# Kernel tuning notes

Hardware: AMD Instinct MI355X
Metric: run time of the kernel (lower is better)

The kernel has to match this reference:

```python
import jax, jax.numpy as jnp
import numpy as np

L_LAYERS = 4
B = 8
PATCH_H = 37
PATCH_W = 37
P = PATCH_H * PATCH_W  # 1369
D = 1024
J = 768
H = 518
W = 518
R_LIST = [1, 3, 5]
K_LIST = [1, 2, 3]
TOPMIN_MIN = 0.0
TOPMIN_MAX = 0.3


def setup_inputs() -> dict:
    key = jax.random.key(0)
    k1, k2 = jax.random.split(key)
    features = jax.random.normal(k1, (L_LAYERS, B, P, D), dtype=jnp.float32)
    cls_tokens = jax.random.normal(k2, (B, J), dtype=jnp.float32)
    return {"features": features, "cls_tokens": cls_tokens}


def _layer_norm_2d(x, eps=1e-5):
    # torch.layer_norm with normalized_shape = (P, D): normalize jointly over last two dims, no affine
    mu = jnp.mean(x, axis=(-2, -1), keepdims=True)
    var = jnp.var(x, axis=(-2, -1), keepdims=True)
    return (x - mu) * jax.lax.rsqrt(var + eps)


def _lnamd(features, r):
    # LNAMD: unfold(r,r, zero pad r//2) + adaptive_avg_pool1d(D*r*r -> D) == per-channel r x r
    # neighborhood mean over the patch grid with zero padding (pool bins are exactly r*r wide).
    if r == 1:
        return features
    l, b, p, d = features.shape
    x = features.reshape(l * b, PATCH_H, PATCH_W, d)
    pad = r // 2
    s = jax.lax.reduce_window(x, 0.0, jax.lax.add, (1, r, r, 1), (1, 1, 1, 1),
                              [(0, 0), (pad, pad), (pad, pad), (0, 0)])
    return (s / float(r * r)).reshape(l, b, p, d)


def _msm(rf, use_remat=False):
    # rf: [L,B,P,D] L2-normalized. Mutual scoring: for each image i, euclidean cdist of its
    # patches to all other images' patches, min over ref patches, mean of [k_min:k_max] smallest.
    l, b, p, d = rf.shape
    k_min = int(TOPMIN_MIN * (b - 1))
    k_max = int(TOPMIN_MAX * (b - 1))
    sq = jnp.sum(rf * rf, axis=-1)  # [L,B,P]

    def per_image(i):
        feat = rf[:, i]  # [L,P,D]
        dots = jnp.einsum('lpd,lbqd->lpbq', feat, rf)  # [L,P,B,P]
        d2 = sq[:, i][:, :, None, None] + sq[:, None, :, :] - 2.0 * dots
        dist = jnp.sqrt(jnp.maximum(d2, 1e-12))
        mind = jnp.min(dist, axis=-1)  # [L,P,B]
        mind = jnp.where(jnp.arange(b)[None, None, :] == i, jnp.inf, mind)  # exclude self
        neg_top = jax.lax.top_k(-mind, k_max)[0]  # k_max smallest distances (ascending)
        sel = -neg_top[..., k_min:k_max]
        return jnp.mean(sel, axis=-1)  # [L,P]

    fn = jax.checkpoint(per_image) if use_remat else per_image
    scores = jax.lax.map(fn, jnp.arange(b))  # [B,L,P]; lax.map keeps one cdist block live at a time
    return jnp.transpose(scores, (1, 0, 2))  # [L,B,P]


def _rscin(sim, scores, top_k):
    # zero out the B-top_k smallest similarities per row (keep top_k largest), row-normalize, reweight
    b = sim.shape[0]
    if top_k < b:
        vals, idx = jax.lax.top_k(sim, top_k)
        masked = jnp.zeros_like(sim).at[jnp.arange(b)[:, None], idx].set(vals)
    else:
        masked = sim
    masked = masked / jnp.sum(masked, axis=-1, keepdims=True)
    return masked @ scores


def _interp_mat(out_len, in_len):
    # bilinear, align_corners=True: src = dst * (in-1)/(out-1); separable 1D interpolation matrix
    pos = jnp.arange(out_len, dtype=jnp.float32) * ((in_len - 1) / (out_len - 1))
    i0 = jnp.clip(jnp.floor(pos).astype(jnp.int32), 0, in_len - 1)
    i1 = jnp.minimum(i0 + 1, in_len - 1)
    w = pos - i0.astype(jnp.float32)
    m = jnp.zeros((out_len, in_len), jnp.float32)
    m = m.at[jnp.arange(out_len), i0].add(1.0 - w)
    m = m.at[jnp.arange(out_len), i1].add(w)
    return m


def _forward(features, cls_tokens, use_remat=False):
    feats = _layer_norm_2d(features)  # [L,B,P,D]
    per_r = []
    for r in R_LIST:
        rf = _lnamd(feats, r)
        rf = rf / jnp.linalg.norm(rf, axis=-1, keepdims=True)
        per_r.append(jnp.mean(_msm(rf, use_remat), axis=0))  # mean over layers -> [B,P]
    scores = jnp.mean(jnp.stack(per_r, axis=0), axis=0)  # [B,P]
    img_scores = jnp.max(scores, axis=1)  # [B]
    cls = cls_tokens / jnp.linalg.norm(cls_tokens, axis=-1, keepdims=True)
    sim = cls @ cls.T  # [B,B]
    final = jnp.mean(jnp.stack([_rscin(sim, img_scores, k) for k in K_LIST], axis=0), axis=0)
    patch = scores.reshape(-1, PATCH_H, PATCH_W)
    mh = _interp_mat(H, PATCH_H)
    mw = _interp_mat(W, PATCH_W)
    pixel = jnp.einsum('Hh,bhw,Ww->bHW', mh, patch, mw)  # [B,H,W]
    return final, pixel


def reference(features, cls_tokens):
    return _forward(features, cls_tokens)
```

## Files before the change

kernel.cpp:

```cpp
#include <hip/hip_runtime.h>
#include <hip/hip_bf16.h>
#include <math.h>

#define L_LAYERS 4
#define BIMG 8
#define PATCH_H 37
#define PATCH_W 37
#define PP 1369
#define DD 1024
#define JJ 768
#define HOUT 518
#define WOUT 518
#define PPAD 1408
#define NPAIR 28

typedef __bf16 bf16x8 __attribute__((ext_vector_type(8)));
typedef float floatx4 __attribute__((ext_vector_type(4)));

__device__ __forceinline__ unsigned short f2bf(float f) {
  unsigned int u = __float_as_uint(f);
  u = u + 0x7fffu + ((u >> 16) & 1u);
  return (unsigned short)(u >> 16);
}

__device__ __forceinline__ void gload_lds16(const unsigned short* gptr,
                                            unsigned short* lptr) {
  __builtin_amdgcn_global_load_lds(
      (const __attribute__((address_space(1))) unsigned int*)gptr,
      (__attribute__((address_space(3))) unsigned int*)lptr, 16, 0, 0);
}

__global__ __launch_bounds__(256) void k1_mu(const float* __restrict__ x,
                                             float* __restrict__ mu_acc) {
  const int lb = blockIdx.y;
  const float* base = x + (size_t)lb * PP * DD;
  const int N4 = PP * DD / 4;
  float s = 0.0f;
  for (int idx = blockIdx.x * 256 + threadIdx.x; idx < N4; idx += gridDim.x * 256) {
    float4 u = *(const float4*)(base + (size_t)idx * 4);
    s += u.x + u.y + u.z + u.w;
  }
  for (int off = 1; off < 64; off <<= 1) s += __shfl_xor(s, off, 64);
  __shared__ float red[4];
  if ((threadIdx.x & 63) == 0) red[threadIdx.x >> 6] = s;
  __syncthreads();
  if (threadIdx.x == 0)
    atomicAdd(&mu_acc[lb], red[0] + red[1] + red[2] + red[3]);
}

__global__ __launch_bounds__(256) void k2_pool(const float* __restrict__ x,
                                               const float* __restrict__ mu_acc,
                                               unsigned short* __restrict__ rf,
                                               int r) {
  const int p  = blockIdx.x;
  const int lb = blockIdx.y;
  const int tid = threadIdx.x;
  const int d0 = tid * 4;
  const size_t outbase = ((size_t)lb * PPAD + p) * DD;
  if (p >= PP) {
    ushort4 z; z.x = 0; z.y = 0; z.z = 0; z.w = 0;
    *(ushort4*)(rf + outbase + d0) = z;
    return;
  }
  const float mu = mu_acc[lb] * (1.0f / ((float)PP * (float)DD));
  const int ph = p / PATCH_W, pw = p % PATCH_W;
  const int pad = r >> 1;
  float s0 = 0, s1 = 0, s2 = 0, s3 = 0;
  int cnt = 0;
  for (int dy = -pad; dy <= pad; dy++) {
    int qh = ph + dy; if (qh < 0 || qh >= PATCH_H) continue;
    for (int dx = -pad; dx <= pad; dx++) {
      int qw = pw + dx; if (qw < 0 || qw >= PATCH_W) continue;
      cnt++;
      const float* src = x + ((size_t)lb * PP + qh * PATCH_W + qw) * DD + d0;
      float4 u = *(const float4*)src;
      s0 += u.x; s1 += u.y; s2 += u.z; s3 += u.w;
    }
  }
  const float cm = (float)cnt * mu;
  s0 -= cm; s1 -= cm; s2 -= cm; s3 -= cm;
  float sq = s0 * s0 + s1 * s1 + s2 * s2 + s3 * s3;
  for (int off = 1; off < 64; off <<= 1) sq += __shfl_xor(sq, off, 64);
  __shared__ float red[4];
  if ((tid & 63) == 0) red[tid >> 6] = sq;
  __syncthreads();
  const float tot = red[0] + red[1] + red[2] + red[3];
  const float rn = rsqrtf(tot);
  ushort4 o;
  o.x = f2bf(s0 * rn); o.y = f2bf(s1 * rn); o.z = f2bf(s2 * rn); o.w = f2bf(s3 * rn);
  *(ushort4*)(rf + outbase + d0) = o;
}

__global__ __launch_bounds__(256) void k3_pairdots(const unsigned short* __restrict__ rf,
                                                   unsigned int* __restrict__ mind) {
  const int l = blockIdx.z / NPAIR;
  int rem = blockIdx.z % NPAIR;
  int i = 0, span = BIMG - 1;
  while (rem >= span) { rem -= span; span--; i++; }
  const int j = i + 1 + rem;

  const int rowbase = blockIdx.x * 128;
  const int colbase = blockIdx.y * 128;
  const unsigned short* A  = rf + ((size_t)(l * BIMG + i) * PPAD + rowbase) * DD;
  const unsigned short* Bp = rf + ((size_t)(l * BIMG + j) * PPAD + colbase) * DD;

  __shared__ __align__(16) unsigned short lA[128 * 32];
  __shared__ __align__(16) unsigned short lB[128 * 32];

  const int tid  = threadIdx.x;
  const int lane = tid & 63;
  const int wave = tid >> 6;
  const int lrow = lane & 15;
  const int quad = lane >> 4;
  const int wr = (wave >> 1) * 64;
  const int wc = (wave & 1) * 64;

  floatx4 acc[4][4];
#pragma unroll
  for (int a = 0; a < 4; a++)
#pragma unroll
    for (int b = 0; b < 4; b++) acc[a][b] = (floatx4){0.f, 0.f, 0.f, 0.f};

  const int srow   = wave * 32 + (lane >> 2);
  const int schunk = (lane & 3) * 8;
  const unsigned short* gA0 = A  + (size_t)srow * DD + schunk;
  const unsigned short* gA1 = gA0 + (size_t)16 * DD;
  const unsigned short* gB0 = Bp + (size_t)srow * DD + schunk;
  const unsigned short* gB1 = gB0 + (size_t)16 * DD;
  unsigned short* lA0 = lA + wave * 1024;
  unsigned short* lB0 = lB + wave * 1024;

  for (int k0 = 0; k0 < DD; k0 += 32) {
    __syncthreads();
    gload_lds16(gA0 + k0, lA0);
    gload_lds16(gA1 + k0, lA0 + 512);
    gload_lds16(gB0 + k0, lB0);
    gload_lds16(gB1 + k0, lB0 + 512);
    __syncthreads();
    bf16x8 af[4], bfv[4];
#pragma unroll
    for (int mt = 0; mt < 4; mt++)
      af[mt] = *(const bf16x8*)(lA + (wr + mt * 16 + lrow) * 32 + quad * 8);
#pragma unroll
    for (int ct = 0; ct < 4; ct++)
      bfv[ct] = *(const bf16x8*)(lB + (wc + ct * 16 + lrow) * 32 + quad * 8);
#pragma unroll
    for (int mt = 0; mt < 4; mt++)
#pragma unroll
      for (int ct = 0; ct < 4; ct++)
        acc[mt][ct] = __builtin_amdgcn_mfma_f32_16x16x32_bf16(af[mt], bfv[ct],
                                                              acc[mt][ct], 0, 0, 0);
  }

  unsigned int* mrow = mind + ((size_t)(l * BIMG + i) * BIMG + j) * PP;
  unsigned int* mcol = mind + ((size_t)(l * BIMG + j) * BIMG + i) * PP;

#pragma unroll
  for (int mt = 0; mt < 4; mt++) {
#pragma unroll
    for (int reg = 0; reg < 4; reg++) {
      const int gr = rowbase + wr + mt * 16 + quad * 4 + reg;
      float v = -1e30f;
#pragma unroll
      for (int ct = 0; ct < 4; ct++) {
        const int gc = colbase + wc + ct * 16 + lrow;
        if (gc < PP) v = fmaxf(v, acc[mt][ct][reg]);
      }
      for (int off = 1; off < 16; off <<= 1) v = fmaxf(v, __shfl_xor(v, off, 64));
      if (lrow == 0 && gr < PP && v > -1e29f)
        atomicMax(mrow + gr, __float_as_uint(v + 2.0f));
    }
  }
#pragma unroll
  for (int ct = 0; ct < 4; ct++) {
    const int gc = colbase + wc + ct * 16 + lrow;
    float v = -1e30f;
#pragma unroll
    for (int mt = 0; mt < 4; mt++) {
      const int grb = rowbase + wr + mt * 16 + quad * 4;
#pragma unroll
      for (int reg = 0; reg < 4; reg++)
        if (grb + reg < PP) v = fmaxf(v, acc[mt][ct][reg]);
    }
    for (int off = 16; off < 64; off <<= 1) v = fmaxf(v, __shfl_xor(v, off, 64));
    if (quad == 0 && gc < PP && v > -1e29f)
      atomicMax(mcol + gc, __float_as_uint(v + 2.0f));
  }
}

__global__ void k4_scores(const unsigned int* __restrict__ mind,
                          float* __restrict__ scores) {
  const int idx = blockIdx.x * 256 + threadIdx.x;
  if (idx >= BIMG * PP) return;
  const int i = idx / PP, p = idx % PP;
  float accum = 0.0f;
  for (int l = 0; l < L_LAYERS; l++) {
    float m1 = 1e30f, m2 = 1e30f;
    for (int b = 0; b < BIMG; b++) {
      if (b == i) continue;
      const unsigned int enc = mind[((size_t)(l * BIMG + i) * BIMG + b) * PP + p];
      const float dot = __uint_as_float(enc) - 2.0f;
      const float d2 = fmaxf(2.0f - 2.0f * dot, 1e-12f);
      const float dist = sqrtf(d2);
      if (dist < m1) { m2 = m1; m1 = dist; }
      else if (dist < m2) { m2 = dist; }
    }
    accum += 0.5f * (m1 + m2);
  }
  scores[idx] += accum * (1.0f / (float)(L_LAYERS * 3));
}

__global__ void k5_imgmax(const float* __restrict__ scores, float* __restrict__ img) {
  const int i = blockIdx.x;
  float m = -1e30f;
  for (int p = threadIdx.x; p < PP; p += 256) m = fmaxf(m, scores[i * PP + p]);
  for (int off = 1; off < 64; off <<= 1) m = fmaxf(m, __shfl_xor(m, off, 64));
  __shared__ float red[4];
  if ((threadIdx.x & 63) == 0) red[threadIdx.x >> 6] = m;
  __syncthreads();
  if (threadIdx.x == 0)
    img[i] = fmaxf(fmaxf(red[0], red[1]), fmaxf(red[2], red[3]));
}

__global__ void k6_final(const float* __restrict__ cls,
                         const float* __restrict__ img,
                         float* __restrict__ out) {
  __shared__ float norms[BIMG];
  __shared__ float sim[BIMG][BIMG];
  const int t = threadIdx.x;
  if (t < BIMG) {
    float s = 0;
    for (int d = 0; d < JJ; d++) { float v = cls[t * JJ + d]; s += v * v; }
    norms[t] = sqrtf(s);
  }
  __syncthreads();
  {
    const int ii = t >> 3, jj = t & 7;
    float s = 0;
    for (int d = 0; d < JJ; d++) s += cls[ii * JJ + d] * cls[jj * JJ + d];
    sim[ii][jj] = s / (norms[ii] * norms[jj]);
  }
  __syncthreads();
  if (t < BIMG) {
    float v[8]; int id[8];
    for (int a = 0; a < 8; a++) { v[a] = sim[t][a]; id[a] = a; }
    for (int a = 0; a < 8; a++) {
      int best = a;
      for (int b = a + 1; b < 8; b++) if (v[b] > v[best]) best = b;
      float tv = v[a]; v[a] = v[best]; v[best] = tv;
      int ti = id[a]; id[a] = id[best]; id[best] = ti;
    }
    float res = 0;
    for (int k = 1; k <= 3; k++) {
      float num = 0, den = 0;
      for (int a = 0; a < k; a++) { num += v[a] * img[id[a]]; den += v[a]; }
      res += num / den;
    }
    out[t] = res * (1.0f / 3.0f);
  }
}

__global__ void k7_pixel(const float* __restrict__ scores,
                         float* __restrict__ out) {
  const int idx = blockIdx.x * 256 + threadIdx.x;
  if (idx >= BIMG * HOUT * WOUT) return;
  const int b = idx / (HOUT * WOUT);
  const int rem = idx % (HOUT * WOUT);
  const int Y = rem / WOUT, X = rem % WOUT;
  const float sy = (float)(PATCH_H - 1) / (float)(HOUT - 1);
  const float sx = (float)(PATCH_W - 1) / (float)(WOUT - 1);
  float py = (float)Y * sy;
  float px = (float)X * sx;
  int y0 = (int)floorf(py); y0 = min(max(y0, 0), PATCH_H - 1);
  int x0 = (int)floorf(px); x0 = min(max(x0, 0), PATCH_W - 1);
  const int y1 = min(y0 + 1, PATCH_H - 1);
  const int x1 = min(x0 + 1, PATCH_W - 1);
  const float wy = py - (float)y0, wx = px - (float)x0;
  const float* sc = scores + (size_t)b * PP;
  const float v =
      (1.f - wy) * ((1.f - wx) * sc[y0 * PATCH_W + x0] + wx * sc[y0 * PATCH_W + x1]) +
      wy         * ((1.f - wx) * sc[y1 * PATCH_W + x0] + wx * sc[y1 * PATCH_W + x1]);
  out[8 + idx] = v;
}

extern "C" void kernel_launch(void* const* d_in, const int* in_sizes, int n_in,
                              void* d_out, int out_size, void* d_ws, size_t ws_size,
                              hipStream_t stream) {
  const float* feat = (const float*)d_in[0];
  const float* cls  = (const float*)d_in[1];
  float* out = (float*)d_out;

  char* ws = (char*)d_ws;
  size_t off = 0;
  unsigned short* rf = (unsigned short*)(ws + off);
  off += (size_t)L_LAYERS * BIMG * PPAD * DD * 2;
  unsigned int* mind = (unsigned int*)(ws + off);
  off += (size_t)L_LAYERS * BIMG * BIMG * PP * 4;
  float* scores = (float*)(ws + off);
  off += (size_t)BIMG * PP * 4;
  float* mu_acc = (float*)(ws + off);
  off += 32 * 4;
  float* img = (float*)(ws + off);
  off += 8 * 4;

  hipMemsetAsync(mu_acc, 0, 32 * 4, stream);
  hipMemsetAsync(scores, 0, (size_t)BIMG * PP * 4, stream);
  k1_mu<<<dim3(43, 32), 256, 0, stream>>>(feat, mu_acc);

  const int rlist[3] = {1, 3, 5};
  for (int ri = 0; ri < 3; ri++) {
    k2_pool<<<dim3(PPAD, 32), 256, 0, stream>>>(feat, mu_acc, rf, rlist[ri]);
    hipMemsetAsync(mind, 0, (size_t)L_LAYERS * BIMG * BIMG * PP * 4, stream);
    k3_pairdots<<<dim3(11, 11, L_LAYERS * NPAIR), 256, 0, stream>>>(rf, mind);
    k4_scores<<<(BIMG * PP + 255) / 256, 256, 0, stream>>>(mind, scores);
  }
  k5_imgmax<<<8, 256, 0, stream>>>(scores, img);
  k6_final<<<1, 64, 0, stream>>>(cls, img, out);
  k7_pixel<<<(BIMG * HOUT * WOUT + 255) / 256, 256, 0, stream>>>(scores, out);
}
```

Measured before the change: 2.927 ms.

## Quantize normalized features to FP8 e4m3 and use fp8 MFMA for pair dots

Normalized pooled features are now stored as FP8 e4m3, scaled by 16, instead of bf16. The Gram-matrix kernel uses fp8 MFMA with 64-wide K steps and XOR-swizzled LDS. Each row's quantized squared norm is stored, so distances are rebuilt as n_i + n_j - 2dot from the actual quantized values. This halves feature bandwidth and LDS traffic and doubles MFMA throughput, at the cost of lower precision in the nearest-neighbour distances.

New measurement: 2.594 ms. -11.4%, faster.

```diff
diff --git a/kernel.cpp b/kernel.cpp
--- a/kernel.cpp
+++ b/kernel.cpp
@@ -14,17 +14,31 @@
 #define PPAD 1408
 #define NPAIR 28
 
-typedef __bf16 bf16x8 __attribute__((ext_vector_type(8)));
 typedef float floatx4 __attribute__((ext_vector_type(4)));
 
-__device__ __forceinline__ unsigned short f2bf(float f) {
-  unsigned int u = __float_as_uint(f);
-  u = u + 0x7fffu + ((u >> 16) & 1u);
-  return (unsigned short)(u >> 16);
-}
-
-__device__ __forceinline__ void gload_lds16(const unsigned short* gptr,
-                                            unsigned short* lptr) {
+__device__ __forceinline__ unsigned int f2e4m3(float v) {
+  unsigned int b = __float_as_uint(v);
+  unsigned int sign = (b >> 24) & 0x80u;
+  float mag = fabsf(v);
+  unsigned int code;
+  if (mag >= 0.015625f) {
+    unsigned int mb = __float_as_uint(mag);
+    mb = mb + 0x0007ffffu + ((mb >> 20) & 1u);
+    code = (((mb >> 23) - 120u) << 3) | ((mb >> 20) & 7u);
+  } else {
+    code = (unsigned int)__float2int_rn(mag * 512.0f);
+  }
+  return code | sign;
+}
+__device__ __forceinline__ float e4m3tof(unsigned int c) {
+  unsigned int em = c & 0x7fu;
+  float m;
+  if (em >= 8u) m = __uint_as_float((((em >> 3) + 120u) << 23) | ((em & 7u) << 20));
+  else          m = (float)em * 0.001953125f;
+  return (c & 0x80u) ? -m : m;
+}
+
+__device__ __forceinline__ void gload_lds16(const void* gptr, void* lptr) {
   __builtin_amdgcn_global_load_lds(
       (const __attribute__((address_space(1))) unsigned int*)gptr,
       (__attribute__((address_space(3))) unsigned int*)lptr, 16, 0, 0);
@@ -50,7 +64,8 @@
 
 __global__ __launch_bounds__(256) void k2_pool(const float* __restrict__ x,
                                                const float* __restrict__ mu_acc,
-                                               unsigned short* __restrict__ rf,
+                                               unsigned char* __restrict__ rf,
+                                               float* __restrict__ nrm,
                                                int r) {
   const int p  = blockIdx.x;
   const int lb = blockIdx.y;
@@ -58,8 +73,9 @@
   const int d0 = tid * 4;
   const size_t outbase = ((size_t)lb * PPAD + p) * DD;
   if (p >= PP) {
-    ushort4 z; z.x = 0; z.y = 0; z.z = 0; z.w = 0;
-    *(ushort4*)(rf + outbase + d0) = z;
+    uchar4 z; z.x = 0; z.y = 0; z.z = 0; z.w = 0;
+    *(uchar4*)(rf + outbase + d0) = z;
+    if (tid == 0) nrm[(size_t)lb * PPAD + p] = 0.0f;
     return;
   }
   const float mu = mu_acc[lb] * (1.0f / ((float)PP * (float)DD));
@@ -84,14 +100,24 @@
   __shared__ float red[4];
   if ((tid & 63) == 0) red[tid >> 6] = sq;
   __syncthreads();
-  const float tot = red[0] + red[1] + red[2] + red[3];
-  const float rn = rsqrtf(tot);
-  ushort4 o;
-  o.x = f2bf(s0 * rn); o.y = f2bf(s1 * rn); o.z = f2bf(s2 * rn); o.w = f2bf(s3 * rn);
-  *(ushort4*)(rf + outbase + d0) = o;
-}
-
-__global__ __launch_bounds__(256) void k3_pairdots(const unsigned short* __restrict__ rf,
+  const float rn16 = rsqrtf(red[0] + red[1] + red[2] + red[3]) * 16.0f;
+  unsigned int c0 = f2e4m3(s0 * rn16), c1 = f2e4m3(s1 * rn16);
+  unsigned int c2 = f2e4m3(s2 * rn16), c3 = f2e4m3(s3 * rn16);
+  uchar4 o; o.x = (unsigned char)c0; o.y = (unsigned char)c1;
+  o.z = (unsigned char)c2; o.w = (unsigned char)c3;
+  *(uchar4*)(rf + outbase + d0) = o;
+  float q0 = e4m3tof(c0), q1 = e4m3tof(c1), q2 = e4m3tof(c2), q3 = e4m3tof(c3);
+  float nq = q0 * q0 + q1 * q1 + q2 * q2 + q3 * q3;
+  for (int off = 1; off < 64; off <<= 1) nq += __shfl_xor(nq, off, 64);
+  __syncthreads();
+  if ((tid & 63) == 0) red[tid >> 6] = nq;
+  __syncthreads();
+  if (tid == 0)
+    nrm[(size_t)lb * PPAD + p] = red[0] + red[1] + red[2] + red[3];
+}
+
+__global__ __launch_bounds__(256) void k3_pairdots(const unsigned char* __restrict__ rf,
+                                                   const float* __restrict__ nrm,
                                                    unsigned int* __restrict__ mind) {
   const int l = blockIdx.z / NPAIR;
   int rem = blockIdx.z % NPAIR;
@@ -101,11 +127,11 @@
 
   const int rowbase = blockIdx.x * 128;
   const int colbase = blockIdx.y * 128;
-  const unsigned short* A  = rf + ((size_t)(l * BIMG + i) * PPAD + rowbase) * DD;
-  const unsigned short* Bp = rf + ((size_t)(l * BIMG + j) * PPAD + colbase) * DD;
-
-  __shared__ __align__(16) unsigned short lA[128 * 32];
-  __shared__ __align__(16) unsigned short lB[128 * 32];
+  const unsigned char* A  = rf + ((size_t)(l * BIMG + i) * PPAD + rowbase) * DD;
+  const unsigned char* Bp = rf + ((size_t)(l * BIMG + j) * PPAD + colbase) * DD;
+
+  __shared__ __align__(16) unsigned char lA[128 * 64];
+  __shared__ __align__(16) unsigned char lB[128 * 64];
 
   const int tid  = threadIdx.x;
   const int lane = tid & 63;
@@ -121,39 +147,66 @@
 #pragma unroll
     for (int b = 0; b < 4; b++) acc[a][b] = (floatx4){0.f, 0.f, 0.f, 0.f};
 
-  const int srow   = wave * 32 + (lane >> 2);
-  const int schunk = (lane & 3) * 8;
-  const unsigned short* gA0 = A  + (size_t)srow * DD + schunk;
-  const unsigned short* gA1 = gA0 + (size_t)16 * DD;
-  const unsigned short* gB0 = Bp + (size_t)srow * DD + schunk;
-  const unsigned short* gB1 = gB0 + (size_t)16 * DD;
-  unsigned short* lA0 = lA + wave * 1024;
-  unsigned short* lB0 = lB + wave * 1024;
-
-  for (int k0 = 0; k0 < DD; k0 += 32) {
+  const int r0  = wave * 32 + (lane >> 2);
+  const int gsw = (lane & 3) ^ ((lane >> 3) & 3);
+  const unsigned char* gA0 = A  + (size_t)r0 * DD + gsw * 16;
+  const unsigned char* gA1 = gA0 + (size_t)16 * DD;
+  const unsigned char* gB0 = Bp + (size_t)r0 * DD + gsw * 16;
+  const unsigned char* gB1 = gB0 + (size_t)16 * DD;
+  unsigned char* dA0 = lA + wave * 2048;
+  unsigned char* dA1 = dA0 + 1024;
+  unsigned char* dB0 = lB + wave * 2048;
+  unsigned char* dB1 = dB0 + 1024;
+
+  const int swf = (lrow >> 1) & 3;
+  const int sub8 = (quad & 1) * 8;
+  int rowoffA[4], rowoffB[4];
+#pragma unroll
+  for (int t = 0; t < 4; t++) {
+    rowoffA[t] = (wr + t * 16 + lrow) * 64 + sub8;
+    rowoffB[t] = (wc + t * 16 + lrow) * 64 + sub8;
+  }
+
+  for (int k0 = 0; k0 < DD; k0 += 64) {
     __syncthreads();
-    gload_lds16(gA0 + k0, lA0);
-    gload_lds16(gA1 + k0, lA0 + 512);
-    gload_lds16(gB0 + k0, lB0);
-    gload_lds16(gB1 + k0, lB0 + 512);
+    gload_lds16(gA0 + k0, dA0);
+    gload_lds16(gA1 + k0, dA1);
+    gload_lds16(gB0 + k0, dB0);
+    gload_lds16(gB1 + k0, dB1);
     __syncthreads();
-    bf16x8 af[4], bfv[4];
-#pragma unroll
-    for (int mt = 0; mt < 4; mt++)
-      af[mt] = *(const bf16x8*)(lA + (wr + mt * 16 + lrow) * 32 + quad * 8);
-#pragma unroll
-    for (int ct = 0; ct < 4; ct++)
-      bfv[ct] = *(const bf16x8*)(lB + (wc + ct * 16 + lrow) * 32 + quad * 8);
-#pragma unroll
-    for (int mt = 0; mt < 4; mt++)
+#pragma unroll
+    for (int ks = 0; ks < 2; ks++) {
+      const int gfrag = (((ks << 1) + (quad >> 1)) ^ swf) * 16;
+      long af[4], bfv[4];
+#pragma unroll
+      for (int mt = 0; mt < 4; mt++)
+        af[mt] = *(const long*)(lA + rowoffA[mt] + gfrag);
 #pragma unroll
       for (int ct = 0; ct < 4; ct++)
-        acc[mt][ct] = __builtin_amdgcn_mfma_f32_16x16x32_bf16(af[mt], bfv[ct],
-                                                              acc[mt][ct], 0, 0, 0);
-  }
-
+        bfv[ct] = *(const long*)(lB + rowoffB[ct] + gfrag);
+#pragma unroll
+      for (int mt = 0; mt < 4; mt++)
+#pragma unroll
+        for (int ct = 0; ct < 4; ct++)
+          acc[mt][ct] = __builtin_amdgcn_mfma_f32_16x16x32_fp8_fp8(
+              af[mt], bfv[ct], acc[mt][ct], 0, 0, 0);
+    }
+  }
+
+  const float* nI = nrm + (size_t)(l * BIMG + i) * PPAD;
+  const float* nJ = nrm + (size_t)(l * BIMG + j) * PPAD;
   unsigned int* mrow = mind + ((size_t)(l * BIMG + i) * BIMG + j) * PP;
   unsigned int* mcol = mind + ((size_t)(l * BIMG + j) * BIMG + i) * PP;
+
+  float nj[4];
+#pragma unroll
+  for (int ct = 0; ct < 4; ct++) nj[ct] = nJ[colbase + wc + ct * 16 + lrow];
+  float ni[4][4];
+#pragma unroll
+  for (int mt = 0; mt < 4; mt++)
+#pragma unroll
+    for (int reg = 0; reg < 4; reg++)
+      ni[mt][reg] = nI[rowbase + wr + mt * 16 + quad * 4 + reg];
 
 #pragma unroll
   for (int mt = 0; mt < 4; mt++) {
@@ -164,11 +217,11 @@
 #pragma unroll
       for (int ct = 0; ct < 4; ct++) {
         const int gc = colbase + wc + ct * 16 + lrow;
-        if (gc < PP) v = fmaxf(v, acc[mt][ct][reg]);
+        if (gc < PP) v = fmaxf(v, 2.0f * acc[mt][ct][reg] - nj[ct]);
       }
       for (int off = 1; off < 16; off <<= 1) v = fmaxf(v, __shfl_xor(v, off, 64));
-      if (lrow == 0 && gr < PP && v > -1e29f)
-        atomicMax(mrow + gr, __float_as_uint(v + 2.0f));
+      if (lrow == 0 && gr < PP)
+        atomicMax(mrow + gr, __float_as_uint(v + 1024.0f));
     }
   }
 #pragma unroll
@@ -180,27 +233,29 @@
       const int grb = rowbase + wr + mt * 16 + quad * 4;
 #pragma unroll
       for (int reg = 0; reg < 4; reg++)
-        if (grb + reg < PP) v = fmaxf(v, acc[mt][ct][reg]);
+        if (grb + reg < PP) v = fmaxf(v, 2.0f * acc[mt][ct][reg] - ni[mt][reg]);
     }
     for (int off = 16; off < 64; off <<= 1) v = fmaxf(v, __shfl_xor(v, off, 64));
-    if (quad == 0 && gc < PP && v > -1e29f)
-      atomicMax(mcol + gc, __float_as_uint(v + 2.0f));
+    if (quad == 0 && gc < PP)
+      atomicMax(mcol + gc, __float_as_uint(v + 1024.0f));
   }
 }
 
 __global__ void k4_scores(const unsigned int* __restrict__ mind,
+                          const float* __restrict__ nrm,
                           float* __restrict__ scores) {
   const int idx = blockIdx.x * 256 + threadIdx.x;
   if (idx >= BIMG * PP) return;
   const int i = idx / PP, p = idx % PP;
   float accum = 0.0f;
   for (int l = 0; l < L_LAYERS; l++) {
+    const float n_own = nrm[(size_t)(l * BIMG + i) * PPAD + p];
     float m1 = 1e30f, m2 = 1e30f;
     for (int b = 0; b < BIMG; b++) {
       if (b == i) continue;
       const unsigned int enc = mind[((size_t)(l * BIMG + i) * BIMG + b) * PP + p];
-      const float dot = __uint_as_float(enc) - 2.0f;
-      const float d2 = fmaxf(2.0f - 2.0f * dot, 1e-12f);
+      const float val = __uint_as_float(enc) - 1024.0f;
+      const float d2 = fmaxf((n_own - val) * (1.0f / 256.0f), 1e-12f);
       const float dist = sqrtf(d2);
       if (dist < m1) { m2 = m1; m1 = dist; }
       else if (dist < m2) { m2 = dist; }
@@ -292,10 +347,12 @@
 
   char* ws = (char*)d_ws;
   size_t off = 0;
-  unsigned short* rf = (unsigned short*)(ws + off);
-  off += (size_t)L_LAYERS * BIMG * PPAD * DD * 2;
+  unsigned char* rf = (unsigned char*)(ws + off);
+  off += (size_t)L_LAYERS * BIMG * PPAD * DD;
   unsigned int* mind = (unsigned int*)(ws + off);
   off += (size_t)L_LAYERS * BIMG * BIMG * PP * 4;
+  float* nrm = (float*)(ws + off);
+  off += (size_t)L_LAYERS * BIMG * PPAD * 4;
   float* scores = (float*)(ws + off);
   off += (size_t)BIMG * PP * 4;
   float* mu_acc = (float*)(ws + off);
@@ -309,10 +366,10 @@
 
   const int rlist[3] = {1, 3, 5};
   for (int ri = 0; ri < 3; ri++) {
-    k2_pool<<<dim3(PPAD, 32), 256, 0, stream>>>(feat, mu_acc, rf, rlist[ri]);
+    k2_pool<<<dim3(PPAD, 32), 256, 0, stream>>>(feat, mu_acc, rf, nrm, rlist[ri]);
     hipMemsetAsync(mind, 0, (size_t)L_LAYERS * BIMG * BIMG * PP * 4, stream);
-    k3_pairdots<<<dim3(11, 11, L_LAYERS * NPAIR), 256, 0, stream>>>(rf, mind);
-    k4_scores<<<(BIMG * PP + 255) / 256, 256, 0, stream>>>(mind, scores);
+    k3_pairdots<<<dim3(11, 11, L_LAYERS * NPAIR), 256, 0, stream>>>(rf, nrm, mind);
+    k4_scores<<<(BIMG * PP + 255) / 256, 256, 0, stream>>>(mind, nrm, scores);
   }
   k5_imgmax<<<8, 256, 0, stream>>>(scores, img);
   k6_final<<<1, 64, 0, stream>>>(cls, img, out);
```
